# Kernel tuning notes

Measured on AMD Instinct MI355X. Metric: run time of the kernel, lower is better.

## Reference

```python
import jax, jax.numpy as jnp
import numpy as np

N = 20000       # num_nodes
B = 4           # batch
D = 32          # input_dim
OUT = 64        # output_dim
S = 2           # n_supports
E = 640000      # edges per support (avg degree 32)
MAX_STEP = 3
M = MAX_STEP * S + 1  # num_metrics = 7


def setup_inputs() -> dict:
    key = jax.random.key(0)
    k = jax.random.split(key, 6)
    inputs = jax.random.normal(k[0], (B, N, D), dtype=jnp.float32)
    edge_src = jax.random.randint(k[1], (S, E), 0, N, dtype=jnp.int32)
    edge_dst = jax.random.randint(k[2], (S, E), 0, N, dtype=jnp.int32)
    # ~1/deg scaled values so the diffusion recurrence stays numerically tame
    edge_vals = jax.random.uniform(k[3], (S, E), dtype=jnp.float32) / 32.0
    W = jax.random.normal(k[4], (OUT, D * M), dtype=jnp.float32) * 0.05
    bias = jnp.zeros((OUT,), dtype=jnp.float32)
    return dict(inputs=inputs, edge_vals=edge_vals, W=W, bias=bias,
                edge_src=edge_src, edge_dst=edge_dst)


def _spmm(vals, src, dst, x):
    # y[i] = sum_{edges (i<-j)} vals * x[j]  == support.mm(x) for COO support
    return jax.ops.segment_sum(vals[:, None] * x[src], dst, num_segments=N)


def reference(inputs, edge_vals, W, bias, edge_src, edge_dst):
    b, n, d = inputs.shape
    # x0: [N, D*B], batch fastest (matches permute([1,2,0]).reshape(n,-1))
    x0 = jnp.transpose(inputs, (1, 2, 0)).reshape(n, -1)
    xs = [x0]
    for s in range(S):
        v, sr, ds = edge_vals[s], edge_src[s], edge_dst[s]
        x1 = _spmm(v, sr, ds, x0)
        xs.append(x1)
        for _ in range(2, MAX_STEP + 1):
            x2 = 2.0 * _spmm(v, sr, ds, x1) - x0
            xs.append(x2)
            # NOTE: faithful to source aliasing quirk — x0 is mutated here,
            # so the next support starts from the mutated x0.
            x1, x0 = x2, x1
    x = jnp.stack(xs, 0)                       # [M, N, D*B]
    x = x.reshape(-1, n, d, b)                 # [M, N, D, B]
    x = jnp.transpose(x, (3, 1, 2, 0))         # [B, N, D, M]
    x = x.reshape(b, n, -1)                    # [B, N, D*M], M fastest
    return x @ W.T + bias                      # [B, N, OUT]
```

## Files before the change

### kernel.cpp

```cpp
#include <hip/hip_runtime.h>

#define N_NODES 20000
#define BATCH   4
#define DIN     32
#define DOUT    64
#define MSTEPS  7
#define ROW     128
#define NROW    896
#define NROWU   448
#define PLN     656
#define NT      79
#define KB2     (2 * NT)
#define CHUNK   2048
#define SLOT    12288
#define WSLOT   3584
#define RGRID   (N_NODES / 4)

typedef short  short8 __attribute__((ext_vector_type(8)));
typedef float  f32x4  __attribute__((ext_vector_type(4)));

__device__ __forceinline__ unsigned short f2bf(float f) {
    unsigned u = __float_as_uint(f);
    unsigned r = u + 0x7fff + ((u >> 16) & 1);
    return (unsigned short)(r >> 16);
}
__device__ __forceinline__ float bf_lo(unsigned p) { return __uint_as_float(p << 16); }
__device__ __forceinline__ float bf_hi(unsigned p) { return __uint_as_float(p & 0xffff0000u); }

__global__ void transpose_in_k(const float* __restrict__ in, unsigned short* __restrict__ xs) {
    int tid = blockIdx.x * 256 + threadIdx.x;
    if (tid >= N_NODES * ROW) return;
    int b = tid & 3;
    int d = (tid >> 2) & 31;
    int n = tid >> 7;
    xs[(size_t)n * NROW + d * 4 + b] = f2bf(in[(b * N_NODES + n) * DIN + d]);
}


__global__ void p00_init_k(int* __restrict__ cursor) {
    int t = threadIdx.x;
    if (t < KB2) cursor[t] = t * SLOT;
}

__global__ void __launch_bounds__(256) p2_part_k(const int* __restrict__ src,
                                                 const int* __restrict__ dst,
                                                 const float* __restrict__ vals,
                                                 int* __restrict__ cursor,
                                                 uint2* __restrict__ staged, int E) {
    __shared__ int lhist[KB2];
    __shared__ int lbase[KB2];
    __shared__ int gbase[KB2];
    __shared__ int sc[256];
    __shared__ uint2 buf[CHUNK];
    __shared__ unsigned short kk[CHUNK];
    int t = threadIdx.x;
    int base = blockIdx.x * CHUNK;
    int nval = min(CHUNK, 2 * E - base);
    for (int i = t; i < KB2; i += 256) lhist[i] = 0;
    __syncthreads();
    int k[CHUNK / 256], pos[CHUNK / 256];
    uint2 pay[CHUNK / 256];
#pragma unroll
    for (int j = 0; j < CHUNK / 256; ++j) {
        int i = j * 256 + t;
        int e = base + i;
        if (i < nval) {
            int s = (e >= E) ? 1 : 0;
            int d = dst[e];
            pay[j] = make_uint2((unsigned)src[e] | ((unsigned)f2bf(vals[e]) << 16),
                                (unsigned)d);
            k[j] = s * NT + (d >> 8);
            pos[j] = atomicAdd(&lhist[k[j]], 1);
        } else k[j] = -1;
    }
    __syncthreads();
    int v = (t < KB2) ? lhist[t] : 0;
    sc[t] = v;
    __syncthreads();
    for (int off = 1; off < 256; off <<= 1) {
        int a = (t >= off) ? sc[t - off] : 0;
        __syncthreads();
        sc[t] += a;
        __syncthreads();
    }
    if (t < KB2) lbase[t] = sc[t] - v;
    __syncthreads();
    if (t < KB2 && lhist[t]) gbase[t] = atomicAdd(&cursor[t], lhist[t]);
#pragma unroll
    for (int j = 0; j < CHUNK / 256; ++j) {
        if (k[j] >= 0) {
            int slot = lbase[k[j]] + pos[j];
            buf[slot] = pay[j];
            kk[slot] = (unsigned short)k[j];
        }
    }
    __syncthreads();
#pragma unroll
    for (int j = 0; j < CHUNK / 256; ++j) {
        int i = j * 256 + t;
        if (i < nval) {
            int b = kk[i];
            staged[gbase[b] + (i - lbase[b])] = buf[i];
        }
    }
}

__global__ void __launch_bounds__(256) p3_fine_k(const uint2* __restrict__ staged,
                                                 const int* __restrict__ cursor,
                                                 int2* __restrict__ row_desc,
                                                 unsigned* __restrict__ csr) {
    __shared__ int lhist[64];
    __shared__ int sc[64];
    __shared__ int lcur[64];
    __shared__ int before_sh;
    int bb = blockIdx.x;
    int b = bb >> 2, sub = bb & 3;
    int s = b / NT, tile = b - s * NT;
    int w0loc = sub * 64;
    int seg0 = b * SLOT;
    int len = cursor[b] - seg0;
    int t = threadIdx.x;
    if (t < 64) lhist[t] = 0;
    if (t == 0) before_sh = 0;
    __syncthreads();
    for (int i = t; i < len; i += 256) {
        int dl = (int)(staged[seg0 + i].y & 255) - w0loc;
        if (dl >= 0 && dl < 64) atomicAdd(&lhist[dl], 1);
    }
    __syncthreads();
    int cntr = (t < 64) ? lhist[t] : 0;
    int pl = (cntr + 7) & ~7;
    if (t < 64) sc[t] = pl;
    __syncthreads();
    for (int off = 1; off < 64; off <<= 1) {
        int a = (t < 64 && t >= off) ? sc[t - off] : 0;
        __syncthreads();
        if (t < 64) sc[t] += a;
        __syncthreads();
    }
    int wbase = bb * WSLOT;
    if (t < 64) {
        int excl = sc[t] - pl;
        lcur[t] = wbase + excl;
        int nd = tile * 256 + w0loc + t;
        if (nd < N_NODES) row_desc[s * N_NODES + nd] = make_int2(wbase + excl, pl);
    }
    __syncthreads();
    for (int i = t; i < len; i += 256) {
        uint2 u = staged[seg0 + i];
        int dl = (int)(u.y & 255) - w0loc;
        if (dl >= 0 && dl < 64) {
            int p = atomicAdd(&lcur[dl], 1);
            csr[p] = u.x;
        }
    }
    if (t < 64) {
        int excl = sc[t] - pl;
        for (int i = cntr; i < pl; ++i) csr[wbase + excl + i] = 0u;
    }
}

__device__ __forceinline__ void spmm_core(const int2* __restrict__ rdesc,
                                          const unsigned* __restrict__ csr,
                                          const unsigned* __restrict__ xb,
                                          const unsigned* __restrict__ xprevb,
                                          unsigned* __restrict__ yb,
                                          float alpha, int node, int lane) {
    int2 rd = rdesc[node];
    int start = rd.x, end = rd.x + rd.y;
    float l0 = 0.f, h0 = 0.f, l1 = 0.f, h1 = 0.f;
    float l2 = 0.f, h2 = 0.f, l3 = 0.f, h3 = 0.f;
    for (int e = start; e < end; e += 8) {
        unsigned c0 = csr[e],     c1 = csr[e + 1], c2 = csr[e + 2], c3 = csr[e + 3];
        unsigned c4 = csr[e + 4], c5 = csr[e + 5], c6 = csr[e + 6], c7 = csr[e + 7];
        unsigned p0 = xb[(size_t)(c0 & 0xffffu) * NROWU + lane];
        unsigned p1 = xb[(size_t)(c1 & 0xffffu) * NROWU + lane];
        unsigned p2 = xb[(size_t)(c2 & 0xffffu) * NROWU + lane];
        unsigned p3 = xb[(size_t)(c3 & 0xffffu) * NROWU + lane];
        unsigned p4 = xb[(size_t)(c4 & 0xffffu) * NROWU + lane];
        unsigned p5 = xb[(size_t)(c5 & 0xffffu) * NROWU + lane];
        unsigned p6 = xb[(size_t)(c6 & 0xffffu) * NROWU + lane];
        unsigned p7 = xb[(size_t)(c7 & 0xffffu) * NROWU + lane];
        float v0 = bf_hi(c0), v1 = bf_hi(c1), v2 = bf_hi(c2), v3 = bf_hi(c3);
        float v4 = bf_hi(c4), v5 = bf_hi(c5), v6 = bf_hi(c6), v7 = bf_hi(c7);
        l0 = fmaf(v0, bf_lo(p0), l0);  h0 = fmaf(v0, bf_hi(p0), h0);
        l1 = fmaf(v1, bf_lo(p1), l1);  h1 = fmaf(v1, bf_hi(p1), h1);
        l2 = fmaf(v2, bf_lo(p2), l2);  h2 = fmaf(v2, bf_hi(p2), h2);
        l3 = fmaf(v3, bf_lo(p3), l3);  h3 = fmaf(v3, bf_hi(p3), h3);
        l0 = fmaf(v4, bf_lo(p4), l0);  h0 = fmaf(v4, bf_hi(p4), h0);
        l1 = fmaf(v5, bf_lo(p5), l1);  h1 = fmaf(v5, bf_hi(p5), h1);
        l2 = fmaf(v6, bf_lo(p6), l2);  h2 = fmaf(v6, bf_hi(p6), h2);
        l3 = fmaf(v7, bf_lo(p7), l3);  h3 = fmaf(v7, bf_hi(p7), h3);
    }
    float r0 = alpha * ((l0 + l1) + (l2 + l3));
    float r1 = alpha * ((h0 + h1) + (h2 + h3));
    if (xprevb) {
        unsigned pp = xprevb[(size_t)node * NROWU + lane];
        r0 -= bf_lo(pp);
        r1 -= bf_hi(pp);
    }
    yb[(size_t)node * NROWU + lane] = (unsigned)f2bf(r0) | ((unsigned)f2bf(r1) << 16);
}

__global__ void __launch_bounds__(256) spmm_row_k(const int2* __restrict__ rdesc,
                                                  const unsigned* __restrict__ csr,
                                                  const unsigned short* __restrict__ x,
                                                  const unsigned short* __restrict__ xprev,
                                                  unsigned short* __restrict__ y, float alpha) {
    int node = __builtin_amdgcn_readfirstlane(blockIdx.x * 4 + (threadIdx.x >> 6));
    int lane = threadIdx.x & 63;
    spmm_core(rdesc, csr, (const unsigned*)x, (const unsigned*)xprev, (unsigned*)y,
              alpha, node, lane);
}

__global__ void __launch_bounds__(256) spmm_dual_k(const int2* __restrict__ rdA,
                                                   const int2* __restrict__ rdB,
                                                   const unsigned* __restrict__ csr,
                                                   const unsigned short* __restrict__ x,
                                                   const unsigned short* __restrict__ xprevA,
                                                   unsigned short* __restrict__ yA,
                                                   unsigned short* __restrict__ yB) {
    int bid = blockIdx.x;
    int second = (bid >= RGRID) ? 1 : 0;
    int node = __builtin_amdgcn_readfirstlane((bid - second * RGRID) * 4 + (threadIdx.x >> 6));
    int lane = threadIdx.x & 63;
    const int2* rd = second ? rdB : rdA;
    const unsigned* xprevb = second ? nullptr : (const unsigned*)xprevA;
    unsigned* yb = second ? (unsigned*)yB : (unsigned*)yA;
    float alpha = second ? 1.0f : 2.0f;
    spmm_core(rd, csr, (const unsigned*)x, xprevb, yb, alpha, node, lane);
}

__global__ void __launch_bounds__(256) epilogue_mfma_k(const unsigned short* __restrict__ xs,
                                                       const float* __restrict__ W,
                                                       const float* __restrict__ bias,
                                                       float* __restrict__ out) {
    __shared__ unsigned short Alds[28 * PLN];
    int tid = threadIdx.x;
    int lane = tid & 63, ot = tid >> 6;
    int col = lane & 15, quad = lane >> 4;
    int o = ot * 16 + col;

    short8 bfrag[MSTEPS];
#pragma unroll
    for (int m = 0; m < MSTEPS; ++m) {
        short8 bf;
#pragma unroll
        for (int j = 0; j < 8; ++j)
            bf[j] = (short)f2bf(W[o * 224 + (quad * 8 + j) * 7 + m]);
        bfrag[m] = bf;
    }
    float bo = bias[o];

    int n0 = blockIdx.x * 16;
    const uint4* src = (const uint4*)(xs + (size_t)n0 * NROW);
#pragma unroll
    for (int it = 0; it < 7; ++it) {
        int idx = tid + it * 256;
        uint4 q = src[idx];
        int r    = idx / 112;
        int off8 = idx - r * 112;
        int m    = off8 >> 4;
        int d0   = (off8 & 15) * 2;
        unsigned vals[4] = {q.x, q.y, q.z, q.w};
#pragma unroll
        for (int h = 0; h < 4; ++h) {
            int dd = d0 + (h >> 1);
            int bA = (2 * h) & 3, bB = (2 * h + 1) & 3;
            Alds[(bA * 7 + m) * PLN + r * 40 + dd] = (unsigned short)(vals[h] & 0xffffu);
            Alds[(bB * 7 + m) * PLN + r * 40 + dd] = (unsigned short)(vals[h] >> 16);
        }
    }
    __syncthreads();

    f32x4 acc[BATCH];
#pragma unroll
    for (int b = 0; b < BATCH; ++b)
        acc[b] = (f32x4){bo, bo, bo, bo};

#pragma unroll
    for (int m = 0; m < MSTEPS; ++m) {
#pragma unroll
        for (int b = 0; b < BATCH; ++b) {
            short8 a = *(const short8*)&Alds[(b * 7 + m) * PLN + col * 40 + quad * 8];
            acc[b] = __builtin_amdgcn_mfma_f32_16x16x32_bf16(a, bfrag[m], acc[b], 0, 0, 0);
        }
    }

#pragma unroll
    for (int b = 0; b < BATCH; ++b) {
#pragma unroll
        for (int reg = 0; reg < 4; ++reg) {
            int n = n0 + quad * 4 + reg;
            out[((size_t)b * N_NODES + n) * DOUT + o] = acc[b][reg];
        }
    }
}

extern "C" void kernel_launch(void* const* d_in, const int* in_sizes, int n_in,
                              void* d_out, int out_size, void* d_ws, size_t ws_size,
                              hipStream_t stream) {
    const float* inputs    = (const float*)d_in[0];
    const float* edge_vals = (const float*)d_in[1];
    const float* W         = (const float*)d_in[2];
    const float* bias      = (const float*)d_in[3];
    const int*   edge_src  = (const int*)d_in[4];
    const int*   edge_dst  = (const int*)d_in[5];
    float* out = (float*)d_out;
    const int E = in_sizes[1] / 2;

    unsigned short* xs = (unsigned short*)d_ws;
    uint2* staged  = (uint2*)(xs + (size_t)N_NODES * NROW);
    unsigned* csr  = (unsigned*)(staged + (size_t)KB2 * SLOT);
    int* cursor    = (int*)(csr + (size_t)4 * KB2 * WSLOT);
    int2* row_desc = (int2*)(cursor + KB2 + 2);

    const int tgrid  = (N_NODES * ROW + 255) / 256;
    const int pgrid  = (2 * E + CHUNK - 1) / CHUNK;
    const int epgrid = N_NODES / 16;

    p00_init_k<<<1, 256, 0, stream>>>(cursor);
    p2_part_k<<<pgrid, 256, 0, stream>>>(edge_src, edge_dst, edge_vals, cursor, staged, E);
    p3_fine_k<<<4 * KB2, 256, 0, stream>>>(staged, cursor, row_desc, csr);

    const int2* rd0 = row_desc;
    const int2* rd1 = row_desc + N_NODES;

    unsigned short* X0 = xs + 0 * ROW;
    unsigned short* X1 = xs + 1 * ROW;
    unsigned short* X2 = xs + 2 * ROW;
    unsigned short* X3 = xs + 3 * ROW;
    unsigned short* X4 = xs + 4 * ROW;
    unsigned short* X5 = xs + 5 * ROW;
    unsigned short* X6 = xs + 6 * ROW;

    transpose_in_k<<<tgrid, 256, 0, stream>>>(inputs, xs);

    spmm_row_k<<<RGRID, 256, 0, stream>>>(rd0, csr, X0, nullptr, X1, 1.0f);
    spmm_row_k<<<RGRID, 256, 0, stream>>>(rd0, csr, X1, X0,      X2, 2.0f);
    spmm_dual_k<<<2 * RGRID, 256, 0, stream>>>(rd0, rd1, csr, X2, X1, X3, X4);
    spmm_row_k<<<RGRID, 256, 0, stream>>>(rd1, csr, X4, X2, X5, 2.0f);
    spmm_row_k<<<RGRID, 256, 0, stream>>>(rd1, csr, X5, X4, X6, 2.0f);

    epilogue_mfma_k<<<epgrid, 256, 0, stream>>>(xs, W, bias, out);
}
```

Before: 238.3 us.

## Split wavefront into half-waves gathering 8-byte rows; fold cursor init into transpose

```diff
diff --git a/kernel.cpp b/kernel.cpp
--- a/kernel.cpp
+++ b/kernel.cpp
@@ -27,8 +27,10 @@
 __device__ __forceinline__ float bf_lo(unsigned p) { return __uint_as_float(p << 16); }
 __device__ __forceinline__ float bf_hi(unsigned p) { return __uint_as_float(p & 0xffff0000u); }
 
-__global__ void transpose_in_k(const float* __restrict__ in, unsigned short* __restrict__ xs) {
+__global__ void transpose_in_k(const float* __restrict__ in, unsigned short* __restrict__ xs,
+                               int* __restrict__ cursor) {
     int tid = blockIdx.x * 256 + threadIdx.x;
+    if (blockIdx.x == 0 && threadIdx.x < KB2) cursor[threadIdx.x] = threadIdx.x * SLOT;
     if (tid >= N_NODES * ROW) return;
     int b = tid & 3;
     int d = (tid >> 2) & 31;
@@ -36,11 +38,6 @@
     xs[(size_t)n * NROW + d * 4 + b] = f2bf(in[(b * N_NODES + n) * DIN + d]);
 }
 
-
-__global__ void p00_init_k(int* __restrict__ cursor) {
-    int t = threadIdx.x;
-    if (t < KB2) cursor[t] = t * SLOT;
-}
 
 __global__ void __launch_bounds__(256) p2_part_k(const int* __restrict__ src,
                                                  const int* __restrict__ dst,
@@ -112,7 +109,6 @@
     __shared__ int lhist[64];
     __shared__ int sc[64];
     __shared__ int lcur[64];
-    __shared__ int before_sh;
     int bb = blockIdx.x;
     int b = bb >> 2, sub = bb & 3;
     int s = b / NT, tile = b - s * NT;
@@ -121,7 +117,6 @@
     int len = cursor[b] - seg0;
     int t = threadIdx.x;
     if (t < 64) lhist[t] = 0;
-    if (t == 0) before_sh = 0;
     __syncthreads();
     for (int i = t; i < len; i += 256) {
         int dl = (int)(staged[seg0 + i].y & 255) - w0loc;
@@ -168,38 +163,54 @@
                                           float alpha, int node, int lane) {
     int2 rd = rdesc[node];
     int start = rd.x, end = rd.x + rd.y;
-    float l0 = 0.f, h0 = 0.f, l1 = 0.f, h1 = 0.f;
-    float l2 = 0.f, h2 = 0.f, l3 = 0.f, h3 = 0.f;
+    int half = lane >> 5;
+    int sub  = lane & 31;
+    float a0 = 0.f, a1 = 0.f, a2 = 0.f, a3 = 0.f;
+    float b0 = 0.f, b1 = 0.f, b2 = 0.f, b3 = 0.f;
+    const uint2* xb2 = (const uint2*)xb;
     for (int e = start; e < end; e += 8) {
         unsigned c0 = csr[e],     c1 = csr[e + 1], c2 = csr[e + 2], c3 = csr[e + 3];
         unsigned c4 = csr[e + 4], c5 = csr[e + 5], c6 = csr[e + 6], c7 = csr[e + 7];
-        unsigned p0 = xb[(size_t)(c0 & 0xffffu) * NROWU + lane];
-        unsigned p1 = xb[(size_t)(c1 & 0xffffu) * NROWU + lane];
-        unsigned p2 = xb[(size_t)(c2 & 0xffffu) * NROWU + lane];
-        unsigned p3 = xb[(size_t)(c3 & 0xffffu) * NROWU + lane];
-        unsigned p4 = xb[(size_t)(c4 & 0xffffu) * NROWU + lane];
-        unsigned p5 = xb[(size_t)(c5 & 0xffffu) * NROWU + lane];
-        unsigned p6 = xb[(size_t)(c6 & 0xffffu) * NROWU + lane];
-        unsigned p7 = xb[(size_t)(c7 & 0xffffu) * NROWU + lane];
-        float v0 = bf_hi(c0), v1 = bf_hi(c1), v2 = bf_hi(c2), v3 = bf_hi(c3);
-        float v4 = bf_hi(c4), v5 = bf_hi(c5), v6 = bf_hi(c6), v7 = bf_hi(c7);
-        l0 = fmaf(v0, bf_lo(p0), l0);  h0 = fmaf(v0, bf_hi(p0), h0);
-        l1 = fmaf(v1, bf_lo(p1), l1);  h1 = fmaf(v1, bf_hi(p1), h1);
-        l2 = fmaf(v2, bf_lo(p2), l2);  h2 = fmaf(v2, bf_hi(p2), h2);
-        l3 = fmaf(v3, bf_lo(p3), l3);  h3 = fmaf(v3, bf_hi(p3), h3);
-        l0 = fmaf(v4, bf_lo(p4), l0);  h0 = fmaf(v4, bf_hi(p4), h0);
-        l1 = fmaf(v5, bf_lo(p5), l1);  h1 = fmaf(v5, bf_hi(p5), h1);
-        l2 = fmaf(v6, bf_lo(p6), l2);  h2 = fmaf(v6, bf_hi(p6), h2);
-        l3 = fmaf(v7, bf_lo(p7), l3);  h3 = fmaf(v7, bf_hi(p7), h3);
-    }
-    float r0 = alpha * ((l0 + l1) + (l2 + l3));
-    float r1 = alpha * ((h0 + h1) + (h2 + h3));
+        unsigned s0 = half ? (c1 & 0xffffu) : (c0 & 0xffffu);
+        unsigned s1 = half ? (c3 & 0xffffu) : (c2 & 0xffffu);
+        unsigned s2 = half ? (c5 & 0xffffu) : (c4 & 0xffffu);
+        unsigned s3 = half ? (c7 & 0xffffu) : (c6 & 0xffffu);
+        uint2 p0 = xb2[(size_t)s0 * (NROWU / 2) + sub];
+        uint2 p1 = xb2[(size_t)s1 * (NROWU / 2) + sub];
+        uint2 p2 = xb2[(size_t)s2 * (NROWU / 2) + sub];
+        uint2 p3 = xb2[(size_t)s3 * (NROWU / 2) + sub];
+        float v0 = half ? bf_hi(c1) : bf_hi(c0);
+        float v1 = half ? bf_hi(c3) : bf_hi(c2);
+        float v2 = half ? bf_hi(c5) : bf_hi(c4);
+        float v3 = half ? bf_hi(c7) : bf_hi(c6);
+        a0 = fmaf(v0, bf_lo(p0.x), a0);  a1 = fmaf(v0, bf_hi(p0.x), a1);
+        a2 = fmaf(v0, bf_lo(p0.y), a2);  a3 = fmaf(v0, bf_hi(p0.y), a3);
+        b0 = fmaf(v1, bf_lo(p1.x), b0);  b1 = fmaf(v1, bf_hi(p1.x), b1);
+        b2 = fmaf(v1, bf_lo(p1.y), b2);  b3 = fmaf(v1, bf_hi(p1.y), b3);
+        a0 = fmaf(v2, bf_lo(p2.x), a0);  a1 = fmaf(v2, bf_hi(p2.x), a1);
+        a2 = fmaf(v2, bf_lo(p2.y), a2);  a3 = fmaf(v2, bf_hi(p2.y), a3);
+        b0 = fmaf(v3, bf_lo(p3.x), b0);  b1 = fmaf(v3, bf_hi(p3.x), b1);
+        b2 = fmaf(v3, bf_lo(p3.y), b2);  b3 = fmaf(v3, bf_hi(p3.y), b3);
+    }
+    float r0 = a0 + b0, r1 = a1 + b1, r2 = a2 + b2, r3 = a3 + b3;
+    r0 += __shfl_xor(r0, 32, 64);
+    r1 += __shfl_xor(r1, 32, 64);
+    r2 += __shfl_xor(r2, 32, 64);
+    r3 += __shfl_xor(r3, 32, 64);
+    r0 *= alpha; r1 *= alpha; r2 *= alpha; r3 *= alpha;
     if (xprevb) {
-        unsigned pp = xprevb[(size_t)node * NROWU + lane];
-        r0 -= bf_lo(pp);
-        r1 -= bf_hi(pp);
-    }
-    yb[(size_t)node * NROWU + lane] = (unsigned)f2bf(r0) | ((unsigned)f2bf(r1) << 16);
+        uint2 pp = ((const uint2*)xprevb)[(size_t)node * (NROWU / 2) + sub];
+        r0 -= bf_lo(pp.x);
+        r1 -= bf_hi(pp.x);
+        r2 -= bf_lo(pp.y);
+        r3 -= bf_hi(pp.y);
+    }
+    if (half == 0) {
+        uint2 po;
+        po.x = (unsigned)f2bf(r0) | ((unsigned)f2bf(r1) << 16);
+        po.y = (unsigned)f2bf(r2) | ((unsigned)f2bf(r3) << 16);
+        ((uint2*)yb)[(size_t)node * (NROWU / 2) + sub] = po;
+    }
 }
 
 __global__ void __launch_bounds__(256) spmm_row_k(const int2* __restrict__ rdesc,
@@ -319,7 +330,8 @@
     const int pgrid  = (2 * E + CHUNK - 1) / CHUNK;
     const int epgrid = N_NODES / 16;
 
-    p00_init_k<<<1, 256, 0, stream>>>(cursor);
+    transpose_in_k<<<tgrid, 256, 0, stream>>>(inputs, xs, cursor);
+
     p2_part_k<<<pgrid, 256, 0, stream>>>(edge_src, edge_dst, edge_vals, cursor, staged, E);
     p3_fine_k<<<4 * KB2, 256, 0, stream>>>(staged, cursor, row_desc, csr);
 
@@ -334,8 +346,6 @@
     unsigned short* X5 = xs + 5 * ROW;
     unsigned short* X6 = xs + 6 * ROW;
 
-    transpose_in_k<<<tgrid, 256, 0, stream>>>(inputs, xs);
-
     spmm_row_k<<<RGRID, 256, 0, stream>>>(rd0, csr, X0, nullptr, X1, 1.0f);
     spmm_row_k<<<RGRID, 256, 0, stream>>>(rd0, csr, X1, X0,      X2, 2.0f);
     spmm_dual_k<<<2 * RGRID, 256, 0, stream>>>(rd0, rd1, csr, X2, X1, X3, X4);
```

New measurement: 247.1 us. 1.04x slower.
